# Kernel optimization log

Measured on AMD Instinct MI355X. Metric: run time of the kernel, lower is better.

## Reference

```python
import jax, jax.numpy as jnp
import numpy as np

# cv2 GrabCut label codes
GC_BGD, GC_FGD, GC_PR_BGD, GC_PR_FGD = 0, 1, 2, 3
ITER_COUNT = 5
GAMMA = 50.0  # smoothness weight (GrabCut's standard gamma)

B, C, H, W = 2, 256, 512, 512


def setup_inputs() -> dict:
    key = jax.random.key(0)
    k1, k2 = jax.random.split(key)
    features = jax.random.normal(k1, (B, C, H, W), dtype=jnp.float32)
    mask = jax.random.randint(k2, (B, H, W), 0, 2, dtype=jnp.int32)
    return {"features": features, "mask": mask}


def _neighbor_mean(a):
    # a: (B,H,W); 4-neighbor mean with edge replication (smoothness/pairwise term)
    p = jnp.pad(a, ((0, 0), (1, 1), (1, 1)), mode="edge")
    return (p[:, :-2, 1:-1] + p[:, 2:, 1:-1] + p[:, 1:-1, :-2] + p[:, 1:-1, 2:]) * 0.25


def reference(features, mask):
    b, c, h, w = features.shape
    # take first 3 channels as pseudo-RGB image, HWC layout
    img = jnp.transpose(features[:, :3], (0, 2, 3, 1))  # (B,H,W,3)
    # cv2.normalize(..., 0, 255, NORM_MINMAX) over the whole array, then uint8 cast
    mn = img.min(axis=(1, 2, 3), keepdims=True)
    mx = img.max(axis=(1, 2, 3), keepdims=True)
    img = jnp.clip(jnp.floor((img - mn) / (mx - mn + 1e-12) * 255.0), 0.0, 255.0)

    # trimap seeding exactly as in the torch module
    tri = jnp.where(mask == 1, GC_PR_FGD, GC_PR_BGD).astype(jnp.int32)
    bh, bw = int(h * 0.1), int(w * 0.1)
    tri = tri.at[:, :bh, :].set(GC_BGD)
    tri = tri.at[:, h - bh:, :].set(GC_BGD)
    tri = tri.at[:, :, :bw].set(GC_BGD)
    tri = tri.at[:, :, w - bw:].set(GC_BGD)
    tri = tri.at[:, int(h * 0.45):int(h * 0.55), int(w * 0.45):int(w * 0.55)].set(GC_FGD)

    fixed = (tri == GC_BGD) | (tri == GC_FGD)          # hard constraints never change
    fixed_fg = (tri == GC_FGD).astype(img.dtype)
    alpha = ((tri == GC_FGD) | (tri == GC_PR_FGD)).astype(img.dtype)  # fg indicator

    # GrabCut surrogate: iteratively (1) refit fg/bg color models from current
    # labeling (GMM step collapsed to per-region mean), (2) relabel probable
    # pixels by unary (color distance) + pairwise (neighbor agreement) energy
    # -- an ICM approximation of the min-cut step.
    for _ in range(ITER_COUNT):
        a4 = alpha[..., None]                                    # (B,H,W,1)
        fg_mean = (img * a4).sum((1, 2)) / (a4.sum((1, 2)) + 1e-6)        # (B,3)
        bg_mean = (img * (1.0 - a4)).sum((1, 2)) / ((1.0 - a4).sum((1, 2)) + 1e-6)
        d_fg = ((img - fg_mean[:, None, None, :]) ** 2).sum(-1)  # (B,H,W)
        d_bg = ((img - bg_mean[:, None, None, :]) ** 2).sum(-1)
        nb = _neighbor_mean(alpha)
        score = d_bg - d_fg + GAMMA * (2.0 * nb - 1.0)           # >0 -> foreground
        new_alpha = (score > 0).astype(img.dtype)
        alpha = jnp.where(fixed, fixed_fg, new_alpha)

    return alpha  # (B,H,W) in {0,1}, float32
```

## Files before the change

kernel.cpp:

```cpp
#include <hip/hip_runtime.h>
#include <stdint.h>
#include <stddef.h>

#pragma clang fp contract(off)

#define HH 512
#define WW 512
#define HW_ 262144
#define FEAT_BSTRIDE (256*HW_)

__device__ __forceinline__ float quantf(float f, float mn, float denom) {
  float v = (f - mn) / denom * 255.0f;
  v = floorf(v);
  return fminf(fmaxf(v, 0.0f), 255.0f);
}

__device__ __forceinline__ bool is_center(int y, int x) {
  return (y >= 230) & (y < 281) & (x >= 230) & (x < 281);
}
__device__ __forceinline__ bool is_border(int y, int x) {
  return (y < 51) | (y >= 461) | (x < 51) | (x >= 461);
}

__device__ __forceinline__ int wsum(int v) {
#pragma unroll
  for (int m = 32; m >= 1; m >>= 1) v += __shfl_xor(v, m);
  return v;
}

__global__ __launch_bounds__(256) void k_minmax(const float* __restrict__ feat,
                                                float2* __restrict__ mm) {
  int blk = blockIdx.x, tid = threadIdx.x;
  int b = blk >> 7, ib = blk & 127;
  const float4* base =
      reinterpret_cast<const float4*>(feat + (size_t)b * FEAT_BSTRIDE) + (size_t)ib * 1536;
  float mn = 3.4e38f, mx = -3.4e38f;
#pragma unroll
  for (int j = 0; j < 6; j++) {
    float4 v = base[tid + j * 256];
    mn = fminf(mn, fminf(fminf(v.x, v.y), fminf(v.z, v.w)));
    mx = fmaxf(mx, fmaxf(fmaxf(v.x, v.y), fmaxf(v.z, v.w)));
  }
  __shared__ float smn[256], smx[256];
  smn[tid] = mn; smx[tid] = mx;
  __syncthreads();
  for (int s = 128; s >= 1; s >>= 1) {
    if (tid < s) {
      smn[tid] = fminf(smn[tid], smn[tid + s]);
      smx[tid] = fmaxf(smx[tid], smx[tid + s]);
    }
    __syncthreads();
  }
  if (tid == 0) mm[blk] = make_float2(smn[0], smx[0]);
}

__global__ __launch_bounds__(256) void k_init(const float* __restrict__ feat,
                                              const int* __restrict__ mask,
                                              const float2* __restrict__ mm,
                                              uint32_t* __restrict__ packed,
                                              uint8_t* __restrict__ alphaA,
                                              int4* __restrict__ totals,
                                              int4* __restrict__ slot0) {
  int blk = blockIdx.x, tid = threadIdx.x;
  int b = blk >> 8;
  __shared__ float smn[128], smx[128];
  if (tid < 128) { float2 v = mm[b * 128 + tid]; smn[tid] = v.x; smx[tid] = v.y; }
  __syncthreads();
  for (int s = 64; s >= 1; s >>= 1) {
    if (tid < s) {
      smn[tid] = fminf(smn[tid], smn[tid + s]);
      smx[tid] = fmaxf(smx[tid], smx[tid + s]);
    }
    __syncthreads();
  }
  float mn = smn[0];
  float denom = (smx[0] - mn) + 1e-12f;

  int pix = blk * 1024 + tid * 4;
  int pb = pix & (HW_ - 1);
  int y = pb >> 9, xb = pb & 511;
  const float* fbp = feat + (size_t)b * FEAT_BSTRIDE;
  float4 cr = *reinterpret_cast<const float4*>(fbp + pb);
  float4 cg = *reinterpret_cast<const float4*>(fbp + HW_ + pb);
  float4 cb = *reinterpret_cast<const float4*>(fbp + 2 * HW_ + pb);
  int4 mk = *reinterpret_cast<const int4*>(mask + pix);
  float rs[4] = {cr.x, cr.y, cr.z, cr.w};
  float gs[4] = {cg.x, cg.y, cg.z, cg.w};
  float bs[4] = {cb.x, cb.y, cb.z, cb.w};
  int mks[4] = {mk.x, mk.y, mk.z, mk.w};
  int a0 = 0, a1 = 0, a2 = 0, a3 = 0, t0 = 0, t1 = 0, t2 = 0;
  uint32_t pkw[4];
  uint32_t aw = 0;
#pragma unroll
  for (int i = 0; i < 4; i++) {
    int r  = (int)quantf(rs[i], mn, denom);
    int g  = (int)quantf(gs[i], mn, denom);
    int bl = (int)quantf(bs[i], mn, denom);
    pkw[i] = (uint32_t)r | ((uint32_t)g << 8) | ((uint32_t)bl << 16);
    int x = xb + i;
    int a;
    if (is_center(y, x)) a = 1;
    else if (is_border(y, x)) a = 0;
    else a = (mks[i] == 1) ? 1 : 0;
    aw |= (uint32_t)a << (8 * i);
    a0 += r * a; a1 += g * a; a2 += bl * a; a3 += a;
    t0 += r; t1 += g; t2 += bl;
  }
  *reinterpret_cast<uint4*>(packed + pix) = make_uint4(pkw[0], pkw[1], pkw[2], pkw[3]);
  *reinterpret_cast<uint32_t*>(alphaA + pix) = aw;

  a0 = wsum(a0); a1 = wsum(a1); a2 = wsum(a2); a3 = wsum(a3);
  t0 = wsum(t0); t1 = wsum(t1); t2 = wsum(t2);
  __shared__ int xw[4][8];
  int wid = tid >> 6, lane = tid & 63;
  if (lane == 0) {
    xw[wid][0] = a0; xw[wid][1] = a1; xw[wid][2] = a2; xw[wid][3] = a3;
    xw[wid][4] = t0; xw[wid][5] = t1; xw[wid][6] = t2;
  }
  __syncthreads();
  if (tid == 0) {
    int s0 = 0, s1 = 0, s2 = 0, s3 = 0, u0 = 0, u1 = 0, u2 = 0;
#pragma unroll
    for (int w = 0; w < 4; w++) {
      s0 += xw[w][0]; s1 += xw[w][1]; s2 += xw[w][2]; s3 += xw[w][3];
      u0 += xw[w][4]; u1 += xw[w][5]; u2 += xw[w][6];
    }
    slot0[blk]  = make_int4(s0, s1, s2, s3);
    totals[blk] = make_int4(u0, u1, u2, 0);
  }
}

__global__ __launch_bounds__(256) void k_relabel(const uint32_t* __restrict__ packed,
                                                 const uint8_t* __restrict__ ain,
                                                 uint8_t* __restrict__ aout,
                                                 const int4* __restrict__ totals,
                                                 const int4* __restrict__ slotIn,
                                                 int4* __restrict__ slotOut,
                                                 float* __restrict__ out,
                                                 int finalIter) {
  int blk = blockIdx.x, tid = threadIdx.x;
  int b = blk >> 8;
  int r0 = (blk & 255) * 2;

  __shared__ uint32_t arowW[4 * 128];
  {
    int row_i = tid >> 6;
    int src_row = r0 - 1 + row_i;
    src_row = src_row < 0 ? 0 : (src_row > 511 ? 511 : src_row);
    reinterpret_cast<uint2*>(arowW)[tid] = *reinterpret_cast<const uint2*>(
        ain + (size_t)b * HW_ + src_row * 512 + (tid & 63) * 8);
  }

  int4 sv = slotIn[b * 256 + tid];
  int4 tv = totals[b * 256 + tid];
  int v0 = wsum(sv.x), v1 = wsum(sv.y), v2 = wsum(sv.z), v3 = wsum(sv.w);
  int v4 = wsum(tv.x), v5 = wsum(tv.y), v6 = wsum(tv.z);
  __shared__ int xw[4][8];
  int wid = tid >> 6, lane = tid & 63;
  if (lane == 0) {
    xw[wid][0] = v0; xw[wid][1] = v1; xw[wid][2] = v2; xw[wid][3] = v3;
    xw[wid][4] = v4; xw[wid][5] = v5; xw[wid][6] = v6;
  }
  __syncthreads();
  int s0 = xw[0][0] + xw[1][0] + xw[2][0] + xw[3][0];
  int s1 = xw[0][1] + xw[1][1] + xw[2][1] + xw[3][1];
  int s2 = xw[0][2] + xw[1][2] + xw[2][2] + xw[3][2];
  int s3 = xw[0][3] + xw[1][3] + xw[2][3] + xw[3][3];
  int s4 = xw[0][4] + xw[1][4] + xw[2][4] + xw[3][4];
  int s5 = xw[0][5] + xw[1][5] + xw[2][5] + xw[3][5];
  int s6 = xw[0][6] + xw[1][6] + xw[2][6] + xw[3][6];
  int cnt = s3;
  float fden = (float)cnt + 1e-6f;
  float bden = (float)(HW_ - cnt) + 1e-6f;
  float f0 = (float)s0 / fden;
  float f1 = (float)s1 / fden;
  float f2 = (float)s2 / fden;
  float g0 = (float)(s4 - s0) / bden;
  float g1 = (float)(s5 - s1) / bden;
  float g2 = (float)(s6 - s2) / bden;

  int lr = tid >> 7;
  int q  = tid & 127;
  int x0 = q * 4;
  int yy = r0 + lr;
  uint32_t uw = arowW[lr * 128 + q];
  uint32_t cw = arowW[(lr + 1) * 128 + q];
  uint32_t dw = arowW[(lr + 2) * 128 + q];
  const uint8_t* arowB = reinterpret_cast<const uint8_t*>(arowW);
  int lfb = arowB[(lr + 1) * 512 + (x0 > 0 ? x0 - 1 : 0)];
  int rtb = arowB[(lr + 1) * 512 + (x0 + 4 < 512 ? x0 + 4 : 511)];

  int pix = b * HW_ + yy * 512 + x0;
  uint4 pk4 = *reinterpret_cast<const uint4*>(packed + pix);
  uint32_t pka[4] = {pk4.x, pk4.y, pk4.z, pk4.w};
  int a0 = 0, a1 = 0, a2 = 0, a3 = 0;
  uint32_t awout = 0;
  float fouts[4];
#pragma unroll
  for (int i = 0; i < 4; i++) {
    uint32_t rgb = pka[i];
    int ri = (int)(rgb & 255u);
    int gi = (int)((rgb >> 8) & 255u);
    int bi = (int)((rgb >> 16) & 255u);
    float i0 = (float)ri, i1 = (float)gi, i2 = (float)bi;
    int up = (int)((uw >> (8 * i)) & 255u);
    int dn = (int)((dw >> (8 * i)) & 255u);
    int lf = (i == 0) ? lfb : (int)((cw >> (8 * (i - 1))) & 255u);
    int rt = (i == 3) ? rtb : (int)((cw >> (8 * (i + 1))) & 255u);
    float nb = (float)(((up + dn) + lf) + rt) * 0.25f;
    float pair = 50.0f * ((2.0f * nb) - 1.0f);
    float t0 = i0 - f0, t1 = i1 - f1, t2 = i2 - f2;
    float df = ((t0 * t0) + (t1 * t1)) + (t2 * t2);
    float u0 = i0 - g0, u1 = i1 - g1, u2 = i2 - g2;
    float db = ((u0 * u0) + (u1 * u1)) + (u2 * u2);
    float score = (db - df) + pair;
    int x = x0 + i;
    int a;
    if (is_center(yy, x)) a = 1;
    else if (is_border(yy, x)) a = 0;
    else a = (score > 0.0f) ? 1 : 0;
    awout |= (uint32_t)a << (8 * i);
    fouts[i] = (float)a;
    a0 += ri * a; a1 += gi * a; a2 += bi * a; a3 += a;
  }
  *reinterpret_cast<uint32_t*>(aout + pix) = awout;
  if (finalIter)
    *reinterpret_cast<float4*>(out + pix) = make_float4(fouts[0], fouts[1], fouts[2], fouts[3]);

  a0 = wsum(a0); a1 = wsum(a1); a2 = wsum(a2); a3 = wsum(a3);
  __syncthreads();
  if (lane == 0) { xw[wid][0] = a0; xw[wid][1] = a1; xw[wid][2] = a2; xw[wid][3] = a3; }
  __syncthreads();
  if (tid == 0) {
    int o0 = xw[0][0] + xw[1][0] + xw[2][0] + xw[3][0];
    int o1 = xw[0][1] + xw[1][1] + xw[2][1] + xw[3][1];
    int o2 = xw[0][2] + xw[1][2] + xw[2][2] + xw[3][2];
    int o3 = xw[0][3] + xw[1][3] + xw[2][3] + xw[3][3];
    slotOut[blk] = make_int4(o0, o1, o2, o3);
  }
}

extern "C" void kernel_launch(void* const* d_in, const int* in_sizes, int n_in,
                              void* d_out, int out_size, void* d_ws, size_t ws_size,
                              hipStream_t stream) {
  const float* feat = (const float*)d_in[0];
  const int*   mask = (const int*)d_in[1];
  float* out = (float*)d_out;

  char* ws = (char*)d_ws;
  uint8_t*  aA     = (uint8_t*)(ws);
  uint8_t*  aB     = (uint8_t*)(ws + 524288);
  float2*   mm     = (float2*)(ws + 1048576);
  int4*     totals = (int4*)(ws + 1050624);
  int4*     slots  = (int4*)(ws + 1058816);
  uint32_t* packed = (uint32_t*)(ws + 1107968);

  k_minmax<<<256, 256, 0, stream>>>(feat, mm);
  k_init<<<512, 256, 0, stream>>>(feat, mask, mm, packed, aA, totals, slots );

  uint8_t* ain = aA;
  uint8_t* aout_buf = aB;
  for (int k = 0; k < 5; k++) {
    k_relabel<<<512, 256, 0, stream>>>(packed, ain, aout_buf, totals,
                                       slots + (size_t)k * 512,
                                       slots + (size_t)(k + 1) * 512,
                                       out, (k == 4) ? 1 : 0);
    uint8_t* tmp = ain; ain = aout_buf; aout_buf = tmp;
  }
}
```

Before: 590.5 us.

## Fuse all GrabCut stages into one persistent kernel with grid barriers

Replaces the seven separate launches (minmax, init, five relabels) with a single kernel of 512 blocks that synchronises through atomic-counter grid barriers. Each block keeps its packed RGB values and trimap codes in registers across iterations, which removes the packed buffer round trip. The min/max pass is folded into the same pass that loads the three channels. The aim is to remove launch gaps and redundant global traffic. In exchange it relies on all 512 blocks being co-resident and adds a memset plus spin-wait barriers.

```diff
diff --git a/kernel.cpp b/kernel.cpp
--- a/kernel.cpp
+++ b/kernel.cpp
@@ -4,81 +4,70 @@
 
 #pragma clang fp contract(off)
 
-#define HH 512
-#define WW 512
 #define HW_ 262144
 #define FEAT_BSTRIDE (256*HW_)
+#define NBLK 512
 
 __device__ __forceinline__ float quantf(float f, float mn, float denom) {
   float v = (f - mn) / denom * 255.0f;
   v = floorf(v);
   return fminf(fmaxf(v, 0.0f), 255.0f);
 }
-
 __device__ __forceinline__ bool is_center(int y, int x) {
   return (y >= 230) & (y < 281) & (x >= 230) & (x < 281);
 }
 __device__ __forceinline__ bool is_border(int y, int x) {
   return (y < 51) | (y >= 461) | (x < 51) | (x >= 461);
 }
-
 __device__ __forceinline__ int wsum(int v) {
 #pragma unroll
   for (int m = 32; m >= 1; m >>= 1) v += __shfl_xor(v, m);
   return v;
 }
-
-__global__ __launch_bounds__(256) void k_minmax(const float* __restrict__ feat,
-                                                float2* __restrict__ mm) {
-  int blk = blockIdx.x, tid = threadIdx.x;
-  int b = blk >> 7, ib = blk & 127;
-  const float4* base =
-      reinterpret_cast<const float4*>(feat + (size_t)b * FEAT_BSTRIDE) + (size_t)ib * 1536;
-  float mn = 3.4e38f, mx = -3.4e38f;
-#pragma unroll
-  for (int j = 0; j < 6; j++) {
-    float4 v = base[tid + j * 256];
-    mn = fminf(mn, fminf(fminf(v.x, v.y), fminf(v.z, v.w)));
-    mx = fmaxf(mx, fmaxf(fmaxf(v.x, v.y), fmaxf(v.z, v.w)));
-  }
-  __shared__ float smn[256], smx[256];
-  smn[tid] = mn; smx[tid] = mx;
-  __syncthreads();
-  for (int s = 128; s >= 1; s >>= 1) {
-    if (tid < s) {
-      smn[tid] = fminf(smn[tid], smn[tid + s]);
-      smx[tid] = fmaxf(smx[tid], smx[tid + s]);
-    }
-    __syncthreads();
-  }
-  if (tid == 0) mm[blk] = make_float2(smn[0], smx[0]);
-}
-
-__global__ __launch_bounds__(256) void k_init(const float* __restrict__ feat,
-                                              const int* __restrict__ mask,
-                                              const float2* __restrict__ mm,
-                                              uint32_t* __restrict__ packed,
-                                              uint8_t* __restrict__ alphaA,
-                                              int4* __restrict__ totals,
-                                              int4* __restrict__ slot0) {
-  int blk = blockIdx.x, tid = threadIdx.x;
-  int b = blk >> 8;
-  __shared__ float smn[128], smx[128];
-  if (tid < 128) { float2 v = mm[b * 128 + tid]; smn[tid] = v.x; smx[tid] = v.y; }
-  __syncthreads();
-  for (int s = 64; s >= 1; s >>= 1) {
-    if (tid < s) {
-      smn[tid] = fminf(smn[tid], smn[tid + s]);
-      smx[tid] = fmaxf(smx[tid], smx[tid + s]);
-    }
-    __syncthreads();
-  }
-  float mn = smn[0];
-  float denom = (smx[0] - mn) + 1e-12f;
-
-  int pix = blk * 1024 + tid * 4;
-  int pb = pix & (HW_ - 1);
-  int y = pb >> 9, xb = pb & 511;
+__device__ __forceinline__ float wminf(float v) {
+#pragma unroll
+  for (int m = 32; m >= 1; m >>= 1) v = fminf(v, __shfl_xor(v, m));
+  return v;
+}
+__device__ __forceinline__ float wmaxf(float v) {
+#pragma unroll
+  for (int m = 32; m >= 1; m >>= 1) v = fmaxf(v, __shfl_xor(v, m));
+  return v;
+}
+
+__device__ __forceinline__ void gbar(unsigned* cnt, int idx) {
+  __syncthreads();
+  if (threadIdx.x == 0) {
+    __threadfence();
+    __hip_atomic_fetch_add(&cnt[idx], 1u, __ATOMIC_RELAXED,
+                           __HIP_MEMORY_SCOPE_AGENT);
+    while (__hip_atomic_load(&cnt[idx], __ATOMIC_RELAXED,
+                             __HIP_MEMORY_SCOPE_AGENT) < NBLK)
+      __builtin_amdgcn_s_sleep(1);
+    __threadfence();
+  }
+  __syncthreads();
+}
+
+__global__ __launch_bounds__(256, 2) void k_grabcut(
+    const float* __restrict__ feat, const int* __restrict__ mask,
+    float* __restrict__ out,
+    uint8_t* __restrict__ aA, uint8_t* __restrict__ aB,
+    float2* __restrict__ mm, int4* __restrict__ totals,
+    int4* __restrict__ slots, unsigned* __restrict__ bar)
+{
+  const int blk = blockIdx.x, tid = threadIdx.x;
+  const int b = blk >> 8;
+  const int r0 = (blk & 255) * 2;
+  const int wid = tid >> 6, lane = tid & 63;
+
+  __shared__ float sA[4], sB[4];
+  __shared__ int xw[4][8];
+  __shared__ uint32_t arowW[512];
+
+  const int pix = blk * 1024 + tid * 4;
+  const int pb = pix & (HW_ - 1);
+  const int y = pb >> 9, xb = pb & 511;
   const float* fbp = feat + (size_t)b * FEAT_BSTRIDE;
   float4 cr = *reinterpret_cast<const float4*>(fbp + pb);
   float4 cg = *reinterpret_cast<const float4*>(fbp + HW_ + pb);
@@ -88,155 +77,172 @@
   float gs[4] = {cg.x, cg.y, cg.z, cg.w};
   float bs[4] = {cb.x, cb.y, cb.z, cb.w};
   int mks[4] = {mk.x, mk.y, mk.z, mk.w};
-  int a0 = 0, a1 = 0, a2 = 0, a3 = 0, t0 = 0, t1 = 0, t2 = 0;
-  uint32_t pkw[4];
-  uint32_t aw = 0;
+
+  float mn = fminf(fminf(fminf(rs[0], rs[1]), fminf(rs[2], rs[3])),
+                   fminf(fminf(gs[0], gs[1]), fminf(gs[2], gs[3])));
+  mn = fminf(mn, fminf(fminf(bs[0], bs[1]), fminf(bs[2], bs[3])));
+  float mx = fmaxf(fmaxf(fmaxf(rs[0], rs[1]), fmaxf(rs[2], rs[3])),
+                   fmaxf(fmaxf(gs[0], gs[1]), fmaxf(gs[2], gs[3])));
+  mx = fmaxf(mx, fmaxf(fmaxf(bs[0], bs[1]), fmaxf(bs[2], bs[3])));
+  mn = wminf(mn); mx = wmaxf(mx);
+  if (lane == 0) { sA[wid] = mn; sB[wid] = mx; }
+  __syncthreads();
+  if (tid == 0)
+    mm[blk] = make_float2(fminf(fminf(sA[0], sA[1]), fminf(sA[2], sA[3])),
+                          fmaxf(fmaxf(sB[0], sB[1]), fmaxf(sB[2], sB[3])));
+
+  uint32_t code = 0;
 #pragma unroll
   for (int i = 0; i < 4; i++) {
-    int r  = (int)quantf(rs[i], mn, denom);
-    int g  = (int)quantf(gs[i], mn, denom);
-    int bl = (int)quantf(bs[i], mn, denom);
-    pkw[i] = (uint32_t)r | ((uint32_t)g << 8) | ((uint32_t)bl << 16);
     int x = xb + i;
-    int a;
-    if (is_center(y, x)) a = 1;
-    else if (is_border(y, x)) a = 0;
-    else a = (mks[i] == 1) ? 1 : 0;
-    aw |= (uint32_t)a << (8 * i);
-    a0 += r * a; a1 += g * a; a2 += bl * a; a3 += a;
-    t0 += r; t1 += g; t2 += bl;
-  }
-  *reinterpret_cast<uint4*>(packed + pix) = make_uint4(pkw[0], pkw[1], pkw[2], pkw[3]);
-  *reinterpret_cast<uint32_t*>(alphaA + pix) = aw;
-
-  a0 = wsum(a0); a1 = wsum(a1); a2 = wsum(a2); a3 = wsum(a3);
-  t0 = wsum(t0); t1 = wsum(t1); t2 = wsum(t2);
-  __shared__ int xw[4][8];
-  int wid = tid >> 6, lane = tid & 63;
-  if (lane == 0) {
-    xw[wid][0] = a0; xw[wid][1] = a1; xw[wid][2] = a2; xw[wid][3] = a3;
-    xw[wid][4] = t0; xw[wid][5] = t1; xw[wid][6] = t2;
-  }
-  __syncthreads();
-  if (tid == 0) {
-    int s0 = 0, s1 = 0, s2 = 0, s3 = 0, u0 = 0, u1 = 0, u2 = 0;
-#pragma unroll
-    for (int w = 0; w < 4; w++) {
-      s0 += xw[w][0]; s1 += xw[w][1]; s2 += xw[w][2]; s3 += xw[w][3];
-      u0 += xw[w][4]; u1 += xw[w][5]; u2 += xw[w][6];
-    }
-    slot0[blk]  = make_int4(s0, s1, s2, s3);
-    totals[blk] = make_int4(u0, u1, u2, 0);
-  }
-}
-
-__global__ __launch_bounds__(256) void k_relabel(const uint32_t* __restrict__ packed,
-                                                 const uint8_t* __restrict__ ain,
-                                                 uint8_t* __restrict__ aout,
-                                                 const int4* __restrict__ totals,
-                                                 const int4* __restrict__ slotIn,
-                                                 int4* __restrict__ slotOut,
-                                                 float* __restrict__ out,
-                                                 int finalIter) {
-  int blk = blockIdx.x, tid = threadIdx.x;
-  int b = blk >> 8;
-  int r0 = (blk & 255) * 2;
-
-  __shared__ uint32_t arowW[4 * 128];
+    uint32_t c2;
+    if (is_center(y, x)) c2 = 1u;
+    else if (is_border(y, x)) c2 = 2u;
+    else c2 = (mks[i] == 1) ? 3u : 0u;
+    code |= c2 << (2 * i);
+  }
+  gbar(bar, 0);
+
   {
-    int row_i = tid >> 6;
-    int src_row = r0 - 1 + row_i;
-    src_row = src_row < 0 ? 0 : (src_row > 511 ? 511 : src_row);
-    reinterpret_cast<uint2*>(arowW)[tid] = *reinterpret_cast<const uint2*>(
-        ain + (size_t)b * HW_ + src_row * 512 + (tid & 63) * 8);
-  }
-
-  int4 sv = slotIn[b * 256 + tid];
-  int4 tv = totals[b * 256 + tid];
-  int v0 = wsum(sv.x), v1 = wsum(sv.y), v2 = wsum(sv.z), v3 = wsum(sv.w);
-  int v4 = wsum(tv.x), v5 = wsum(tv.y), v6 = wsum(tv.z);
-  __shared__ int xw[4][8];
-  int wid = tid >> 6, lane = tid & 63;
-  if (lane == 0) {
-    xw[wid][0] = v0; xw[wid][1] = v1; xw[wid][2] = v2; xw[wid][3] = v3;
-    xw[wid][4] = v4; xw[wid][5] = v5; xw[wid][6] = v6;
-  }
-  __syncthreads();
-  int s0 = xw[0][0] + xw[1][0] + xw[2][0] + xw[3][0];
-  int s1 = xw[0][1] + xw[1][1] + xw[2][1] + xw[3][1];
-  int s2 = xw[0][2] + xw[1][2] + xw[2][2] + xw[3][2];
-  int s3 = xw[0][3] + xw[1][3] + xw[2][3] + xw[3][3];
-  int s4 = xw[0][4] + xw[1][4] + xw[2][4] + xw[3][4];
-  int s5 = xw[0][5] + xw[1][5] + xw[2][5] + xw[3][5];
-  int s6 = xw[0][6] + xw[1][6] + xw[2][6] + xw[3][6];
-  int cnt = s3;
-  float fden = (float)cnt + 1e-6f;
-  float bden = (float)(HW_ - cnt) + 1e-6f;
-  float f0 = (float)s0 / fden;
-  float f1 = (float)s1 / fden;
-  float f2 = (float)s2 / fden;
-  float g0 = (float)(s4 - s0) / bden;
-  float g1 = (float)(s5 - s1) / bden;
-  float g2 = (float)(s6 - s2) / bden;
-
-  int lr = tid >> 7;
-  int q  = tid & 127;
-  int x0 = q * 4;
-  int yy = r0 + lr;
-  uint32_t uw = arowW[lr * 128 + q];
-  uint32_t cw = arowW[(lr + 1) * 128 + q];
-  uint32_t dw = arowW[(lr + 2) * 128 + q];
-  const uint8_t* arowB = reinterpret_cast<const uint8_t*>(arowW);
-  int lfb = arowB[(lr + 1) * 512 + (x0 > 0 ? x0 - 1 : 0)];
-  int rtb = arowB[(lr + 1) * 512 + (x0 + 4 < 512 ? x0 + 4 : 511)];
-
-  int pix = b * HW_ + yy * 512 + x0;
-  uint4 pk4 = *reinterpret_cast<const uint4*>(packed + pix);
-  uint32_t pka[4] = {pk4.x, pk4.y, pk4.z, pk4.w};
-  int a0 = 0, a1 = 0, a2 = 0, a3 = 0;
-  uint32_t awout = 0;
-  float fouts[4];
-#pragma unroll
-  for (int i = 0; i < 4; i++) {
-    uint32_t rgb = pka[i];
-    int ri = (int)(rgb & 255u);
-    int gi = (int)((rgb >> 8) & 255u);
-    int bi = (int)((rgb >> 16) & 255u);
-    float i0 = (float)ri, i1 = (float)gi, i2 = (float)bi;
-    int up = (int)((uw >> (8 * i)) & 255u);
-    int dn = (int)((dw >> (8 * i)) & 255u);
-    int lf = (i == 0) ? lfb : (int)((cw >> (8 * (i - 1))) & 255u);
-    int rt = (i == 3) ? rtb : (int)((cw >> (8 * (i + 1))) & 255u);
-    float nb = (float)(((up + dn) + lf) + rt) * 0.25f;
-    float pair = 50.0f * ((2.0f * nb) - 1.0f);
-    float t0 = i0 - f0, t1 = i1 - f1, t2 = i2 - f2;
-    float df = ((t0 * t0) + (t1 * t1)) + (t2 * t2);
-    float u0 = i0 - g0, u1 = i1 - g1, u2 = i2 - g2;
-    float db = ((u0 * u0) + (u1 * u1)) + (u2 * u2);
-    float score = (db - df) + pair;
-    int x = x0 + i;
-    int a;
-    if (is_center(yy, x)) a = 1;
-    else if (is_border(yy, x)) a = 0;
-    else a = (score > 0.0f) ? 1 : 0;
-    awout |= (uint32_t)a << (8 * i);
-    fouts[i] = (float)a;
-    a0 += ri * a; a1 += gi * a; a2 += bi * a; a3 += a;
-  }
-  *reinterpret_cast<uint32_t*>(aout + pix) = awout;
-  if (finalIter)
-    *reinterpret_cast<float4*>(out + pix) = make_float4(fouts[0], fouts[1], fouts[2], fouts[3]);
-
-  a0 = wsum(a0); a1 = wsum(a1); a2 = wsum(a2); a3 = wsum(a3);
-  __syncthreads();
-  if (lane == 0) { xw[wid][0] = a0; xw[wid][1] = a1; xw[wid][2] = a2; xw[wid][3] = a3; }
-  __syncthreads();
-  if (tid == 0) {
-    int o0 = xw[0][0] + xw[1][0] + xw[2][0] + xw[3][0];
-    int o1 = xw[0][1] + xw[1][1] + xw[2][1] + xw[3][1];
-    int o2 = xw[0][2] + xw[1][2] + xw[2][2] + xw[3][2];
-    int o3 = xw[0][3] + xw[1][3] + xw[2][3] + xw[3][3];
-    slotOut[blk] = make_int4(o0, o1, o2, o3);
+    float2 v = mm[b * 256 + tid];
+    float m2 = wminf(v.x), x2 = wmaxf(v.y);
+    if (lane == 0) { sA[wid] = m2; sB[wid] = x2; }
+  }
+  __syncthreads();
+  const float bmn = fminf(fminf(sA[0], sA[1]), fminf(sA[2], sA[3]));
+  const float bmx = fmaxf(fmaxf(sB[0], sB[1]), fmaxf(sB[2], sB[3]));
+  const float denom = (bmx - bmn) + 1e-12f;
+
+  uint32_t pk[4];
+  {
+    uint32_t aw = 0;
+    int a0 = 0, a1 = 0, a2 = 0, a3 = 0, t0 = 0, t1 = 0, t2 = 0;
+#pragma unroll
+    for (int i = 0; i < 4; i++) {
+      int r  = (int)quantf(rs[i], bmn, denom);
+      int g  = (int)quantf(gs[i], bmn, denom);
+      int bl = (int)quantf(bs[i], bmn, denom);
+      pk[i] = (uint32_t)r | ((uint32_t)g << 8) | ((uint32_t)bl << 16);
+      uint32_t c2 = (code >> (2 * i)) & 3u;
+      int a = (c2 == 1u || c2 == 3u) ? 1 : 0;
+      aw |= (uint32_t)a << (8 * i);
+      a0 += r * a; a1 += g * a; a2 += bl * a; a3 += a;
+      t0 += r; t1 += g; t2 += bl;
+    }
+    *reinterpret_cast<uint32_t*>(aA + pix) = aw;
+    a0 = wsum(a0); a1 = wsum(a1); a2 = wsum(a2); a3 = wsum(a3);
+    t0 = wsum(t0); t1 = wsum(t1); t2 = wsum(t2);
+    if (lane == 0) {
+      xw[wid][0] = a0; xw[wid][1] = a1; xw[wid][2] = a2; xw[wid][3] = a3;
+      xw[wid][4] = t0; xw[wid][5] = t1; xw[wid][6] = t2;
+    }
+    __syncthreads();
+    if (tid == 0) {
+      slots[blk] = make_int4(xw[0][0] + xw[1][0] + xw[2][0] + xw[3][0],
+                             xw[0][1] + xw[1][1] + xw[2][1] + xw[3][1],
+                             xw[0][2] + xw[1][2] + xw[2][2] + xw[3][2],
+                             xw[0][3] + xw[1][3] + xw[2][3] + xw[3][3]);
+      totals[blk] = make_int4(xw[0][4] + xw[1][4] + xw[2][4] + xw[3][4],
+                              xw[0][5] + xw[1][5] + xw[2][5] + xw[3][5],
+                              xw[0][6] + xw[1][6] + xw[2][6] + xw[3][6], 0);
+    }
+  }
+  gbar(bar, 1);
+
+  for (int k = 0; k < 5; k++) {
+    const uint8_t* ain = (k & 1) ? aB : aA;
+    uint8_t* aout = (k & 1) ? aA : aB;
+    const int4* slotIn = slots + (size_t)k * NBLK;
+
+    {
+      int row_i = tid >> 6;
+      int src_row = r0 - 1 + row_i;
+      src_row = src_row < 0 ? 0 : (src_row > 511 ? 511 : src_row);
+      reinterpret_cast<uint2*>(arowW)[tid] = *reinterpret_cast<const uint2*>(
+          ain + (size_t)b * HW_ + src_row * 512 + (tid & 63) * 8);
+    }
+    int4 sv = slotIn[b * 256 + tid];
+    int4 tv = totals[b * 256 + tid];
+    int v0 = wsum(sv.x), v1 = wsum(sv.y), v2 = wsum(sv.z), v3 = wsum(sv.w);
+    int v4 = wsum(tv.x), v5 = wsum(tv.y), v6 = wsum(tv.z);
+    if (lane == 0) {
+      xw[wid][0] = v0; xw[wid][1] = v1; xw[wid][2] = v2; xw[wid][3] = v3;
+      xw[wid][4] = v4; xw[wid][5] = v5; xw[wid][6] = v6;
+    }
+    __syncthreads();
+    int s0 = xw[0][0] + xw[1][0] + xw[2][0] + xw[3][0];
+    int s1 = xw[0][1] + xw[1][1] + xw[2][1] + xw[3][1];
+    int s2 = xw[0][2] + xw[1][2] + xw[2][2] + xw[3][2];
+    int s3 = xw[0][3] + xw[1][3] + xw[2][3] + xw[3][3];
+    int s4 = xw[0][4] + xw[1][4] + xw[2][4] + xw[3][4];
+    int s5 = xw[0][5] + xw[1][5] + xw[2][5] + xw[3][5];
+    int s6 = xw[0][6] + xw[1][6] + xw[2][6] + xw[3][6];
+    float fden = (float)s3 + 1e-6f;
+    float bden = (float)(HW_ - s3) + 1e-6f;
+    float f0 = (float)s0 / fden;
+    float f1 = (float)s1 / fden;
+    float f2 = (float)s2 / fden;
+    float g0 = (float)(s4 - s0) / bden;
+    float g1 = (float)(s5 - s1) / bden;
+    float g2 = (float)(s6 - s2) / bden;
+
+    int lr = tid >> 7, q = tid & 127, x0 = q * 4;
+    uint32_t uw = arowW[lr * 128 + q];
+    uint32_t cw = arowW[(lr + 1) * 128 + q];
+    uint32_t dw = arowW[(lr + 2) * 128 + q];
+    const uint8_t* arowB = reinterpret_cast<const uint8_t*>(arowW);
+    int lfb = arowB[(lr + 1) * 512 + (x0 > 0 ? x0 - 1 : 0)];
+    int rtb = arowB[(lr + 1) * 512 + (x0 + 4 < 512 ? x0 + 4 : 511)];
+
+    int aa0 = 0, aa1 = 0, aa2 = 0, aa3 = 0;
+    uint32_t awout = 0;
+    float fouts[4];
+#pragma unroll
+    for (int i = 0; i < 4; i++) {
+      uint32_t rgb = pk[i];
+      int ri = (int)(rgb & 255u);
+      int gi = (int)((rgb >> 8) & 255u);
+      int bi = (int)((rgb >> 16) & 255u);
+      float i0 = (float)ri, i1 = (float)gi, i2 = (float)bi;
+      int up = (int)((uw >> (8 * i)) & 255u);
+      int dn = (int)((dw >> (8 * i)) & 255u);
+      int lf = (i == 0) ? lfb : (int)((cw >> (8 * (i - 1))) & 255u);
+      int rt = (i == 3) ? rtb : (int)((cw >> (8 * (i + 1))) & 255u);
+      float nb = (float)(((up + dn) + lf) + rt) * 0.25f;
+      float pair = 50.0f * ((2.0f * nb) - 1.0f);
+      float d0 = i0 - f0, d1 = i1 - f1, d2 = i2 - f2;
+      float df = ((d0 * d0) + (d1 * d1)) + (d2 * d2);
+      float u0 = i0 - g0, u1 = i1 - g1, u2 = i2 - g2;
+      float db = ((u0 * u0) + (u1 * u1)) + (u2 * u2);
+      float score = (db - df) + pair;
+      uint32_t c2 = (code >> (2 * i)) & 3u;
+      int a;
+      if (c2 == 1u) a = 1;
+      else if (c2 == 2u) a = 0;
+      else a = (score > 0.0f) ? 1 : 0;
+      awout |= (uint32_t)a << (8 * i);
+      fouts[i] = (float)a;
+      aa0 += ri * a; aa1 += gi * a; aa2 += bi * a; aa3 += a;
+    }
+    *reinterpret_cast<uint32_t*>(aout + pix) = awout;
+    if (k == 4) {
+      *reinterpret_cast<float4*>(out + pix) =
+          make_float4(fouts[0], fouts[1], fouts[2], fouts[3]);
+    } else {
+      aa0 = wsum(aa0); aa1 = wsum(aa1); aa2 = wsum(aa2); aa3 = wsum(aa3);
+      __syncthreads();
+      if (lane == 0) {
+        xw[wid][0] = aa0; xw[wid][1] = aa1; xw[wid][2] = aa2; xw[wid][3] = aa3;
+      }
+      __syncthreads();
+      if (tid == 0)
+        slots[(size_t)(k + 1) * NBLK + blk] =
+            make_int4(xw[0][0] + xw[1][0] + xw[2][0] + xw[3][0],
+                      xw[0][1] + xw[1][1] + xw[2][1] + xw[3][1],
+                      xw[0][2] + xw[1][2] + xw[2][2] + xw[3][2],
+                      xw[0][3] + xw[1][3] + xw[2][3] + xw[3][3]);
+      gbar(bar, 2 + k);
+    }
   }
 }
 
@@ -251,20 +257,11 @@
   uint8_t*  aA     = (uint8_t*)(ws);
   uint8_t*  aB     = (uint8_t*)(ws + 524288);
   float2*   mm     = (float2*)(ws + 1048576);
-  int4*     totals = (int4*)(ws + 1050624);
-  int4*     slots  = (int4*)(ws + 1058816);
-  uint32_t* packed = (uint32_t*)(ws + 1107968);
-
-  k_minmax<<<256, 256, 0, stream>>>(feat, mm);
-  k_init<<<512, 256, 0, stream>>>(feat, mask, mm, packed, aA, totals, slots );
-
-  uint8_t* ain = aA;
-  uint8_t* aout_buf = aB;
-  for (int k = 0; k < 5; k++) {
-    k_relabel<<<512, 256, 0, stream>>>(packed, ain, aout_buf, totals,
-                                       slots + (size_t)k * 512,
-                                       slots + (size_t)(k + 1) * 512,
-                                       out, (k == 4) ? 1 : 0);
-    uint8_t* tmp = ain; ain = aout_buf; aout_buf = tmp;
-  }
-}
+  int4*     totals = (int4*)(ws + 1052672);
+  int4*     slots  = (int4*)(ws + 1060864);
+  unsigned* bar    = (unsigned*)(ws + 1101824);
+
+  hipMemsetAsync(bar, 0, 64, stream);
+  k_grabcut<<<NBLK, 256, 0, stream>>>(feat, mask, out, aA, aB, mm, totals,
+                                      slots, bar);
+}
```

After: 814.1 us. 1.38x slower.
